# Performance work log

Hardware: AMD Instinct MI355X
Metric: run time of the kernel (lower is better)

## Reference

```python
import jax, jax.numpy as jnp
import numpy as np

K = 3  # local attention window (kernel_size)


def setup_inputs() -> dict:
    key = jax.random.key(0)
    ks = jax.random.split(key, 10)
    B, C, S = 1, 128, 24
    scale = 1.0 / np.sqrt(C).astype(np.float32)
    x = jax.random.normal(ks[0], (B, C, S, S, S), dtype=jnp.float32)
    wq = jax.random.normal(ks[1], (C, C), dtype=jnp.float32) * scale
    bq = jax.random.normal(ks[2], (C,), dtype=jnp.float32) * 0.01
    wk = jax.random.normal(ks[3], (C, C), dtype=jnp.float32) * scale
    bk = jax.random.normal(ks[4], (C,), dtype=jnp.float32) * 0.01
    wv = jax.random.normal(ks[5], (C, C), dtype=jnp.float32) * scale
    bv = jax.random.normal(ks[6], (C,), dtype=jnp.float32) * 0.01
    rel_h = jax.random.normal(ks[7], (C // 2, K, 1, 1), dtype=jnp.float32)
    rel_w = jax.random.normal(ks[8], (C // 2, 1, K, 1), dtype=jnp.float32)
    rel_d = jax.random.normal(ks[9], (C // 2, 1, 1, K), dtype=jnp.float32)
    return {"x": x, "wq": wq, "bq": bq, "wk": wk, "bk": bk,
            "wv": wv, "bv": bv, "rel_h": rel_h, "rel_w": rel_w, "rel_d": rel_d}


def reference(x, wq, bq, wk, bk, wv, bv, rel_h, rel_w, rel_d):
    B, C, H, W, D = x.shape
    p = (K - 1) // 2
    pad = ((0, 0), (0, 0), (p, K - 1 - p), (p, K - 1 - p), (p, K - 1 - p))
    xp = jnp.pad(x, pad)

    # 1x1x1 Conv3d == per-voxel linear map
    conv1 = lambda y, w, b: jnp.einsum('bchwd,oc->bohwd', y, w) + b[None, :, None, None, None]
    q = conv1(x, wq, bq)          # [B,C,H,W,D]
    kf = conv1(xp, wk, bk)        # padded
    vf = conv1(xp, wv, bv)

    def unfold(y):
        # torch unfold(2,K,1).unfold(3,K,1).unfold(4,K,1) flattened row-major (i,j,l)
        pats = [y[:, :, i:i + H, j:j + W, l:l + D]
                for i in range(K) for j in range(K) for l in range(K)]
        return jnp.stack(pats, axis=-1)  # [B,C,H,W,D,K^3]

    kw = unfold(kf)
    vw = unfold(vf)

    # q^T k per voxel over the K^3 window (num_heads=1 so head split is identity)
    qk = jnp.einsum('bchwd,bchwds->bhwds', q, kw)  # [B,H,W,D,27]

    # Faithful to einsum('bhxytdz,cijk->bhxytijk'): d,z,c are all summed
    # independently -> (sum_d q) * (sum_c rel) broadcast over the window.
    qsum = jnp.sum(q, axis=1)                         # [B,H,W,D]
    bias = rel_h.sum(0) + rel_w.sum(0) + rel_d.sum(0)  # [K,K,K] via broadcast
    qk = qk.reshape(B, H, W, D, K, K, K) + qsum[..., None, None, None] * bias

    attn = jax.nn.softmax(qk.reshape(B, H, W, D, K ** 3), axis=-1)
    out = jnp.einsum('bhwds,bchwds->bhwdc', attn, vw)  # [B,H,W,D,C]
    # torch: [B,1,H,W,D,1,C].reshape(B,-1,H,W,D) -- same row-major flatten here
    return out.reshape(B, -1, H, W, D)
```

## Files before the change

### kernel.cpp

```cpp
#include <hip/hip_runtime.h>
#include <hip/hip_fp16.h>

#define CCH 128
#define SV 24
#define NVOX 13824

typedef unsigned short u16;
typedef unsigned int   u32;

__device__ __forceinline__ void cvt8h(uint4 r, float* f) {
    const __half2* h = (const __half2*)&r;
    const float2 a = __half22float2(h[0]);
    const float2 b = __half22float2(h[1]);
    const float2 c = __half22float2(h[2]);
    const float2 d = __half22float2(h[3]);
    f[0] = a.x; f[1] = a.y; f[2] = b.x; f[3] = b.y;
    f[4] = c.x; f[5] = c.y; f[6] = d.x; f[7] = d.y;
}
__device__ __forceinline__ u32 pack2h(float a, float b) {
    const __half2 h = __floats2half2_rn(a, b);
    return *(const u32*)&h;
}

__global__ __launch_bounds__(256) void proj_kernel(
    const float* __restrict__ x,
    const float* __restrict__ wq, const float* __restrict__ bq,
    const float* __restrict__ wk, const float* __restrict__ bk,
    const float* __restrict__ wv, const float* __restrict__ bv,
    const float* __restrict__ relh, const float* __restrict__ relw,
    const float* __restrict__ reld,
    float* __restrict__ qout, u16* __restrict__ kws, u16* __restrict__ vws,
    float* __restrict__ biasW)
{
    const int m = blockIdx.y;
    const float* __restrict__ w = (m == 0) ? wq : (m == 1) ? wk : wv;
    const float* __restrict__ b = (m == 0) ? bq : (m == 1) ? bk : bv;

    __shared__ float Xs[32][64];
    __shared__ float Ws[32][128];

    const int tid  = threadIdx.x;
    const int vox0 = blockIdx.x * 64;
    const int v0   = (tid & 15) * 4;
    const int o0   = (tid >> 4) * 8;

    const int xc  = tid >> 3;
    const int xv  = (tid & 7) * 4;
    const int wo  = tid >> 1;
    const int wkh = (tid & 1) * 16;

    float acc[4][8] = {{0.f}};

    for (int k0 = 0; k0 < CCH; k0 += 32) {
        {
            const float* src = x + (size_t)(k0 + xc) * NVOX + vox0 + xv;
            const float4 a0 = *(const float4*)src;
            const float4 a1 = *(const float4*)(src + 32);
            *(float4*)&Xs[xc][xv]      = a0;
            *(float4*)&Xs[xc][xv + 32] = a1;
        }
        {
            const float* src = w + (size_t)wo * CCH + k0 + wkh;
            const float4 b0 = *(const float4*)src;
            const float4 b1 = *(const float4*)(src + 4);
            const float4 b2 = *(const float4*)(src + 8);
            const float4 b3 = *(const float4*)(src + 12);
            Ws[wkh + 0][wo] = b0.x;  Ws[wkh + 1][wo] = b0.y;
            Ws[wkh + 2][wo] = b0.z;  Ws[wkh + 3][wo] = b0.w;
            Ws[wkh + 4][wo] = b1.x;  Ws[wkh + 5][wo] = b1.y;
            Ws[wkh + 6][wo] = b1.z;  Ws[wkh + 7][wo] = b1.w;
            Ws[wkh + 8][wo] = b2.x;  Ws[wkh + 9][wo] = b2.y;
            Ws[wkh + 10][wo] = b2.z; Ws[wkh + 11][wo] = b2.w;
            Ws[wkh + 12][wo] = b3.x; Ws[wkh + 13][wo] = b3.y;
            Ws[wkh + 14][wo] = b3.z; Ws[wkh + 15][wo] = b3.w;
        }
        __syncthreads();

#pragma unroll
        for (int k = 0; k < 32; ++k) {
            const float4 xf = *(const float4*)&Xs[k][v0];
            const float4 w0 = *(const float4*)&Ws[k][o0];
            const float4 w1 = *(const float4*)&Ws[k][o0 + 4];
            const float xr[4] = {xf.x, xf.y, xf.z, xf.w};
            const float wr[8] = {w0.x, w0.y, w0.z, w0.w,
                                 w1.x, w1.y, w1.z, w1.w};
#pragma unroll
            for (int vv = 0; vv < 4; ++vv)
#pragma unroll
                for (int oo = 0; oo < 8; ++oo)
                    acc[vv][oo] = fmaf(xr[vv], wr[oo], acc[vv][oo]);
        }
        __syncthreads();
    }

    const float4 bf0 = *(const float4*)(b + o0);
    const float4 bf1 = *(const float4*)(b + o0 + 4);
    const float br[8] = {bf0.x, bf0.y, bf0.z, bf0.w,
                         bf1.x, bf1.y, bf1.z, bf1.w};

#pragma unroll
    for (int vv = 0; vv < 4; ++vv) {
        float r[8];
#pragma unroll
        for (int oo = 0; oo < 8; ++oo) r[oo] = acc[vv][oo] + br[oo];
        const size_t row = (size_t)(vox0 + v0 + vv) * CCH + o0;
        if (m == 0) {
            float4 s0 = {r[0], r[1], r[2], r[3]};
            float4 s1 = {r[4], r[5], r[6], r[7]};
            *(float4*)(qout + row) = s0;
            *(float4*)(qout + row + 4) = s1;
        } else {
            u16* out = (m == 1) ? kws : vws;
            uint4 st = {pack2h(r[0], r[1]), pack2h(r[2], r[3]),
                        pack2h(r[4], r[5]), pack2h(r[6], r[7])};
            *(uint4*)(out + row) = st;
        }
    }

    if (blockIdx.x == 0) {
        if (m == 1 && tid < CCH) {
            const __half hb = __float2half_rn(bk[tid]);
            kws[(size_t)NVOX * CCH + tid] = *(const u16*)&hb;
        }
        if (m == 2 && tid < CCH) {
            const __half hb = __float2half_rn(bv[tid]);
            vws[(size_t)NVOX * CCH + tid] = *(const u16*)&hb;
        }
        if (m == 1 && tid < 27) {
            const int i = tid / 9, j = (tid / 3) % 3, l = tid % 3;
            float s = 0.f;
            for (int c = 0; c < 64; ++c)
                s += relh[c * 3 + i] + relw[c * 3 + j] + reld[c * 3 + l];
            biasW[tid] = s;
        }
    }
}

__device__ __forceinline__ int nbr_off(int h, int w, int d, int s, int ch) {
    const int nh = h + s / 9 - 1;
    const int nw = w + (s / 3) % 3 - 1;
    const int nd = d + s % 3 - 1;
    const bool ok = ((unsigned)nh < (unsigned)SV) &&
                    ((unsigned)nw < (unsigned)SV) &&
                    ((unsigned)nd < (unsigned)SV);
    const int idx = ok ? ((nh * SV + nw) * SV + nd) : NVOX;
    return idx * CCH + ch;
}

__global__ __launch_bounds__(256) void attn_kernel(
    float* __restrict__ qo, const u16* __restrict__ kws,
    const u16* __restrict__ vws, const float* __restrict__ biasW)
{
    const int tid  = threadIdx.x;
    const int lane = tid & 15;
    const int vox  = blockIdx.x * 16 + (tid >> 4);
    const int h    = vox / 576;
    const int rem  = vox - h * 576;
    const int w    = rem / 24;
    const int d    = rem - w * 24;
    const int ch   = lane * 8;

    const float* qrow = qo + (size_t)vox * CCH + ch;
    const float4 q0 = *(const float4*)qrow;
    const float4 q1 = *(const float4*)(qrow + 4);
    const float qr[8] = {q0.x, q0.y, q0.z, q0.w, q1.x, q1.y, q1.z, q1.w};

    float qs = qr[0] + qr[1] + qr[2] + qr[3] + qr[4] + qr[5] + qr[6] + qr[7];
#pragma unroll
    for (int mm = 1; mm < 16; mm <<= 1) qs += __shfl_xor(qs, mm, 64);

    float ps[27];
#pragma unroll
    for (int sb = 0; sb < 27; sb += 9) {
        uint4 kf[9];
#pragma unroll
        for (int j = 0; j < 9; ++j)
            kf[j] = *(const uint4*)(kws + nbr_off(h, w, d, sb + j, ch));
#pragma unroll
        for (int j = 0; j < 9; ++j) {
            float f[8];
            cvt8h(kf[j], f);
            float p = qr[0] * f[0];
            p = fmaf(qr[1], f[1], p); p = fmaf(qr[2], f[2], p);
            p = fmaf(qr[3], f[3], p); p = fmaf(qr[4], f[4], p);
            p = fmaf(qr[5], f[5], p); p = fmaf(qr[6], f[6], p);
            p = fmaf(qr[7], f[7], p);
            ps[sb + j] = p;
        }
    }

#pragma unroll
    for (int mm = 1; mm < 16; mm <<= 1) {
#pragma unroll
        for (int s = 0; s < 27; ++s) ps[s] += __shfl_xor(ps[s], mm, 64);
    }

#pragma unroll
    for (int s = 0; s < 27; ++s) ps[s] = fmaf(qs, biasW[s], ps[s]);

    float mx = ps[0];
#pragma unroll
    for (int s = 1; s < 27; ++s) mx = fmaxf(mx, ps[s]);
    float sum = 0.f;
#pragma unroll
    for (int s = 0; s < 27; ++s) { ps[s] = __expf(ps[s] - mx); sum += ps[s]; }
    const float inv = 1.f / sum;
#pragma unroll
    for (int s = 0; s < 27; ++s) ps[s] *= inv;

    float o[8] = {0.f, 0.f, 0.f, 0.f, 0.f, 0.f, 0.f, 0.f};
#pragma unroll
    for (int sb = 0; sb < 27; sb += 9) {
        uint4 vf[9];
#pragma unroll
        for (int j = 0; j < 9; ++j)
            vf[j] = *(const uint4*)(vws + nbr_off(h, w, d, sb + j, ch));
#pragma unroll
        for (int j = 0; j < 9; ++j) {
            float f[8];
            cvt8h(vf[j], f);
            const float a = ps[sb + j];
#pragma unroll
            for (int e = 0; e < 8; ++e) o[e] = fmaf(a, f[e], o[e]);
        }
    }

    float* dst = qo + (size_t)vox * CCH + ch;
    float4 s0 = {o[0], o[1], o[2], o[3]};
    float4 s1 = {o[4], o[5], o[6], o[7]};
    *(float4*)dst = s0;
    *(float4*)(dst + 4) = s1;
}

extern "C" void kernel_launch(void* const* d_in, const int* in_sizes, int n_in,
                              void* d_out, int out_size, void* d_ws,
                              size_t ws_size, hipStream_t stream)
{
    const float* x    = (const float*)d_in[0];
    const float* wq   = (const float*)d_in[1];
    const float* bq   = (const float*)d_in[2];
    const float* wk   = (const float*)d_in[3];
    const float* bk   = (const float*)d_in[4];
    const float* wv   = (const float*)d_in[5];
    const float* bv   = (const float*)d_in[6];
    const float* relh = (const float*)d_in[7];
    const float* relw = (const float*)d_in[8];
    const float* reld = (const float*)d_in[9];

    u16*   kws   = (u16*)d_ws;
    u16*   vws   = kws + (size_t)(NVOX + 1) * CCH;
    float* biasW = (float*)(vws + (size_t)(NVOX + 1) * CCH);

    dim3 pgrid(NVOX / 64, 3);
    proj_kernel<<<pgrid, 256, 0, stream>>>(x, wq, bq, wk, bk, wv, bv,
                                           relh, relw, reld,
                                           (float*)d_out, kws, vws, biasW);
    attn_kernel<<<NVOX / 16, 256, 0, stream>>>((float*)d_out, kws, vws, biasW);
}
```

Baseline: 107.6 us.

## Tile attention into 4x4x2 voxel blocks with shared-memory K/V halo reuse

Rewrites the attention kernel so each block handles a 4x4x2 voxel tile. The 6x6x4 halo of K and then V is staged into LDS, which replaces 27 separate global gathers per voxel with shared reuse across neighbours. Work is reorganised so threads compute several window scores over full channels and then split the output channels. This adds syncthreads, LDS pressure and fewer blocks (432), and the softmax runs serially on only 32 threads.

```diff
diff --git a/kernel.cpp b/kernel.cpp
--- a/kernel.cpp
+++ b/kernel.cpp
@@ -136,100 +136,153 @@
     }
 }
 
-__device__ __forceinline__ int nbr_off(int h, int w, int d, int s, int ch) {
-    const int nh = h + s / 9 - 1;
-    const int nw = w + (s / 3) % 3 - 1;
-    const int nd = d + s % 3 - 1;
-    const bool ok = ((unsigned)nh < (unsigned)SV) &&
-                    ((unsigned)nw < (unsigned)SV) &&
-                    ((unsigned)nd < (unsigned)SV);
-    const int idx = ok ? ((nh * SV + nw) * SV + nd) : NVOX;
-    return idx * CCH + ch;
-}
+#define KSTR 136
+#define QSTR 132
 
 __global__ __launch_bounds__(256) void attn_kernel(
     float* __restrict__ qo, const u16* __restrict__ kws,
     const u16* __restrict__ vws, const float* __restrict__ biasW)
 {
-    const int tid  = threadIdx.x;
-    const int lane = tid & 15;
-    const int vox  = blockIdx.x * 16 + (tid >> 4);
-    const int h    = vox / 576;
-    const int rem  = vox - h * 576;
-    const int w    = rem / 24;
-    const int d    = rem - w * 24;
-    const int ch   = lane * 8;
-
-    const float* qrow = qo + (size_t)vox * CCH + ch;
-    const float4 q0 = *(const float4*)qrow;
-    const float4 q1 = *(const float4*)(qrow + 4);
-    const float qr[8] = {q0.x, q0.y, q0.z, q0.w, q1.x, q1.y, q1.z, q1.w};
-
-    float qs = qr[0] + qr[1] + qr[2] + qr[3] + qr[4] + qr[5] + qr[6] + qr[7];
-#pragma unroll
-    for (int mm = 1; mm < 16; mm <<= 1) qs += __shfl_xor(qs, mm, 64);
-
-    float ps[27];
-#pragma unroll
-    for (int sb = 0; sb < 27; sb += 9) {
-        uint4 kf[9];
-#pragma unroll
-        for (int j = 0; j < 9; ++j)
-            kf[j] = *(const uint4*)(kws + nbr_off(h, w, d, sb + j, ch));
-#pragma unroll
-        for (int j = 0; j < 9; ++j) {
+    __shared__ u16   KV[144 * KSTR];
+    __shared__ float Qs[32 * QSTR];
+    __shared__ float probs[32 * 27];
+
+    const int tid = threadIdx.x;
+    const int bx  = blockIdx.x;
+    const int th = bx / 72, rb = bx % 72, tw = rb / 12, td = rb % 12;
+    const int h0 = th * 4, w0 = tw * 4, d0 = td * 2;
+
+#pragma unroll
+    for (int it = 0; it < 9; ++it) {
+        const int e   = it * 256 + tid;
+        const int row = e >> 4, seg = e & 15;
+        const int lh = row / 24, rr = row % 24, lw = rr >> 2, ld = rr & 3;
+        const int nh = h0 + lh - 1, nw = w0 + lw - 1, nd = d0 + ld - 1;
+        const bool ok = ((unsigned)nh < 24u) && ((unsigned)nw < 24u) &&
+                        ((unsigned)nd < 24u);
+        const int gv = ok ? ((nh * 24 + nw) * 24 + nd) : NVOX;
+        const uint4 kv = *(const uint4*)(kws + (size_t)gv * CCH + seg * 8);
+        *(uint4*)&KV[row * KSTR + seg * 8] = kv;
+    }
+#pragma unroll
+    for (int it = 0; it < 4; ++it) {
+        const int e = it * 256 + tid;
+        const int v = e >> 5, seg = e & 31;
+        const int gh = h0 + (v >> 3), gw = w0 + ((v >> 1) & 3),
+                  gd = d0 + (v & 1);
+        const int gv = (gh * 24 + gw) * 24 + gd;
+        const float4 qv = *(const float4*)(qo + (size_t)gv * CCH + seg * 4);
+        *(float4*)&Qs[v * QSTR + seg * 4] = qv;
+    }
+    __syncthreads();
+
+    {
+        const int v  = tid & 31;
+        const int s0 = tid >> 5;
+        const int vh = v >> 3, vw = (v >> 1) & 3, vd = v & 1;
+        int r[4];
+#pragma unroll
+        for (int jj = 0; jj < 4; ++jj) {
+            int s = s0 + jj * 8; if (s > 26) s = 26;
+            const int i = s / 9, j = (s / 3) % 3, l = s % 3;
+            r[jj] = (vh + i) * 24 + (vw + j) * 4 + (vd + l);
+        }
+        float acc[4] = {0.f, 0.f, 0.f, 0.f};
+        for (int c = 0; c < 128; c += 8) {
+            const float4 q0 = *(const float4*)&Qs[v * QSTR + c];
+            const float4 q1 = *(const float4*)&Qs[v * QSTR + c + 4];
+            const float qr[8] = {q0.x, q0.y, q0.z, q0.w,
+                                 q1.x, q1.y, q1.z, q1.w};
+#pragma unroll
+            for (int jj = 0; jj < 4; ++jj) {
+                const uint4 kr = *(const uint4*)&KV[r[jj] * KSTR + c];
+                float f[8];
+                cvt8h(kr, f);
+                float p = acc[jj];
+                p = fmaf(qr[0], f[0], p); p = fmaf(qr[1], f[1], p);
+                p = fmaf(qr[2], f[2], p); p = fmaf(qr[3], f[3], p);
+                p = fmaf(qr[4], f[4], p); p = fmaf(qr[5], f[5], p);
+                p = fmaf(qr[6], f[6], p); p = fmaf(qr[7], f[7], p);
+                acc[jj] = p;
+            }
+        }
+#pragma unroll
+        for (int jj = 0; jj < 4; ++jj) {
+            const int s = s0 + jj * 8;
+            if (s < 27) probs[v * 27 + s] = acc[jj];
+        }
+    }
+    __syncthreads();
+
+    if (tid < 32) {
+        const int v = tid;
+        float qsum = 0.f;
+        for (int c = 0; c < 128; c += 4) {
+            const float4 q = *(const float4*)&Qs[v * QSTR + c];
+            qsum += q.x + q.y + q.z + q.w;
+        }
+        float L[27];
+        float mx = -1e30f;
+#pragma unroll
+        for (int s = 0; s < 27; ++s) {
+            L[s] = fmaf(qsum, biasW[s], probs[v * 27 + s]);
+            mx = fmaxf(mx, L[s]);
+        }
+        float sum = 0.f;
+#pragma unroll
+        for (int s = 0; s < 27; ++s) { L[s] = __expf(L[s] - mx); sum += L[s]; }
+        const float inv = 1.f / sum;
+#pragma unroll
+        for (int s = 0; s < 27; ++s) probs[v * 27 + s] = L[s] * inv;
+    }
+#pragma unroll
+    for (int it = 0; it < 9; ++it) {
+        const int e   = it * 256 + tid;
+        const int row = e >> 4, seg = e & 15;
+        const int lh = row / 24, rr = row % 24, lw = rr >> 2, ld = rr & 3;
+        const int nh = h0 + lh - 1, nw = w0 + lw - 1, nd = d0 + ld - 1;
+        const bool ok = ((unsigned)nh < 24u) && ((unsigned)nw < 24u) &&
+                        ((unsigned)nd < 24u);
+        const int gv = ok ? ((nh * 24 + nw) * 24 + nd) : NVOX;
+        const uint4 vv = *(const uint4*)(vws + (size_t)gv * CCH + seg * 8);
+        *(uint4*)&KV[row * KSTR + seg * 8] = vv;
+    }
+    __syncthreads();
+
+    {
+        const int v  = tid & 31;
+        const int cg = tid >> 5;
+        const int c0 = cg * 16;
+        const int vh = v >> 3, vw = (v >> 1) & 3, vd = v & 1;
+        float acc[16];
+#pragma unroll
+        for (int e = 0; e < 16; ++e) acc[e] = 0.f;
+
+#pragma unroll
+        for (int s = 0; s < 27; ++s) {
+            const int i = s / 9, j = (s / 3) % 3, l = s % 3;
+            const int r = (vh + i) * 24 + (vw + j) * 4 + (vd + l);
+            const float a = probs[v * 27 + s];
+            const uint4 w0 = *(const uint4*)&KV[r * KSTR + c0];
+            const uint4 w1 = *(const uint4*)&KV[r * KSTR + c0 + 8];
             float f[8];
-            cvt8h(kf[j], f);
-            float p = qr[0] * f[0];
-            p = fmaf(qr[1], f[1], p); p = fmaf(qr[2], f[2], p);
-            p = fmaf(qr[3], f[3], p); p = fmaf(qr[4], f[4], p);
-            p = fmaf(qr[5], f[5], p); p = fmaf(qr[6], f[6], p);
-            p = fmaf(qr[7], f[7], p);
-            ps[sb + j] = p;
-        }
-    }
-
-#pragma unroll
-    for (int mm = 1; mm < 16; mm <<= 1) {
-#pragma unroll
-        for (int s = 0; s < 27; ++s) ps[s] += __shfl_xor(ps[s], mm, 64);
-    }
-
-#pragma unroll
-    for (int s = 0; s < 27; ++s) ps[s] = fmaf(qs, biasW[s], ps[s]);
-
-    float mx = ps[0];
-#pragma unroll
-    for (int s = 1; s < 27; ++s) mx = fmaxf(mx, ps[s]);
-    float sum = 0.f;
-#pragma unroll
-    for (int s = 0; s < 27; ++s) { ps[s] = __expf(ps[s] - mx); sum += ps[s]; }
-    const float inv = 1.f / sum;
-#pragma unroll
-    for (int s = 0; s < 27; ++s) ps[s] *= inv;
-
-    float o[8] = {0.f, 0.f, 0.f, 0.f, 0.f, 0.f, 0.f, 0.f};
-#pragma unroll
-    for (int sb = 0; sb < 27; sb += 9) {
-        uint4 vf[9];
-#pragma unroll
-        for (int j = 0; j < 9; ++j)
-            vf[j] = *(const uint4*)(vws + nbr_off(h, w, d, sb + j, ch));
-#pragma unroll
-        for (int j = 0; j < 9; ++j) {
-            float f[8];
-            cvt8h(vf[j], f);
-            const float a = ps[sb + j];
-#pragma unroll
-            for (int e = 0; e < 8; ++e) o[e] = fmaf(a, f[e], o[e]);
-        }
-    }
-
-    float* dst = qo + (size_t)vox * CCH + ch;
-    float4 s0 = {o[0], o[1], o[2], o[3]};
-    float4 s1 = {o[4], o[5], o[6], o[7]};
-    *(float4*)dst = s0;
-    *(float4*)(dst + 4) = s1;
+            cvt8h(w0, f);
+#pragma unroll
+            for (int e = 0; e < 8; ++e) acc[e] = fmaf(a, f[e], acc[e]);
+            cvt8h(w1, f);
+#pragma unroll
+            for (int e = 0; e < 8; ++e) acc[8 + e] = fmaf(a, f[e], acc[8 + e]);
+        }
+
+        const int gh = h0 + vh, gw = w0 + vw, gd = d0 + vd;
+        float* dst = qo + (size_t)((gh * 24 + gw) * 24 + gd) * CCH + c0;
+#pragma unroll
+        for (int e = 0; e < 4; ++e) {
+            float4 st = {acc[4 * e], acc[4 * e + 1],
+                         acc[4 * e + 2], acc[4 * e + 3]};
+            *(float4*)(dst + 4 * e) = st;
+        }
+    }
 }
 
 extern "C" void kernel_launch(void* const* d_in, const int* in_sizes, int n_in,
@@ -255,5 +308,5 @@
     proj_kernel<<<pgrid, 256, 0, stream>>>(x, wq, bq, wk, bk, wv, bv,
                                            relh, relw, reld,
                                            (float*)d_out, kws, vws, biasW);
-    attn_kernel<<<NVOX / 16, 256, 0, stream>>>((float*)d_out, kws, vws, biasW);
-}
+    attn_kernel<<<432, 256, 0, stream>>>((float*)d_out, kws, vws, biasW);
+}
```

Measured after the change: 112.1 us. 4.2% more time.

## Split Q and KV projections; compute KV projection with fp16 dot2 instructions

Applied to the files above, without the earlier changes.

The single fused projection kernel becomes two: an fp32 Q projection and a K/V projection. The K/V kernel converts x and the weights to packed half pairs in shared memory and accumulates with v_dot2 (fp16 inputs, fp32 accumulate). It also issues the global loads before the barrier so they overlap with the previous iteration, and pads the shared arrays. This halves LDS traffic and FMA count for K/V, at the cost of an extra kernel launch and fp16 rounding of inputs (the outputs were already stored as fp16).

```diff
diff --git a/kernel.cpp b/kernel.cpp
--- a/kernel.cpp
+++ b/kernel.cpp
@@ -7,6 +7,7 @@
 
 typedef unsigned short u16;
 typedef unsigned int   u32;
+typedef __fp16 h2 __attribute__((ext_vector_type(2)));
 
 __device__ __forceinline__ void cvt8h(uint4 r, float* f) {
     const __half2* h = (const __half2*)&r;
@@ -21,21 +22,16 @@
     const __half2 h = __floats2half2_rn(a, b);
     return *(const u32*)&h;
 }
-
-__global__ __launch_bounds__(256) void proj_kernel(
+__device__ __forceinline__ float fdot2(u32 a, u32 b, float c) {
+    return __builtin_amdgcn_fdot2(__builtin_bit_cast(h2, a),
+                                  __builtin_bit_cast(h2, b), c, false);
+}
+
+__global__ __launch_bounds__(256) void proj_q_kernel(
     const float* __restrict__ x,
     const float* __restrict__ wq, const float* __restrict__ bq,
-    const float* __restrict__ wk, const float* __restrict__ bk,
-    const float* __restrict__ wv, const float* __restrict__ bv,
-    const float* __restrict__ relh, const float* __restrict__ relw,
-    const float* __restrict__ reld,
-    float* __restrict__ qout, u16* __restrict__ kws, u16* __restrict__ vws,
-    float* __restrict__ biasW)
+    float* __restrict__ qout)
 {
-    const int m = blockIdx.y;
-    const float* __restrict__ w = (m == 0) ? wq : (m == 1) ? wk : wv;
-    const float* __restrict__ b = (m == 0) ? bq : (m == 1) ? bk : bv;
-
     __shared__ float Xs[32][64];
     __shared__ float Ws[32][128];
 
@@ -60,7 +56,7 @@
             *(float4*)&Xs[xc][xv + 32] = a1;
         }
         {
-            const float* src = w + (size_t)wo * CCH + k0 + wkh;
+            const float* src = wq + (size_t)wo * CCH + k0 + wkh;
             const float4 b0 = *(const float4*)src;
             const float4 b1 = *(const float4*)(src + 4);
             const float4 b2 = *(const float4*)(src + 8);
@@ -93,6 +89,93 @@
         __syncthreads();
     }
 
+    const float4 bf0 = *(const float4*)(bq + o0);
+    const float4 bf1 = *(const float4*)(bq + o0 + 4);
+    const float br[8] = {bf0.x, bf0.y, bf0.z, bf0.w,
+                         bf1.x, bf1.y, bf1.z, bf1.w};
+
+#pragma unroll
+    for (int vv = 0; vv < 4; ++vv) {
+        const size_t row = (size_t)(vox0 + v0 + vv) * CCH + o0;
+        float4 s0 = {acc[vv][0] + br[0], acc[vv][1] + br[1],
+                     acc[vv][2] + br[2], acc[vv][3] + br[3]};
+        float4 s1 = {acc[vv][4] + br[4], acc[vv][5] + br[5],
+                     acc[vv][6] + br[6], acc[vv][7] + br[7]};
+        *(float4*)(qout + row) = s0;
+        *(float4*)(qout + row + 4) = s1;
+    }
+}
+
+__global__ __launch_bounds__(256) void proj_kv_kernel(
+    const float* __restrict__ x,
+    const float* __restrict__ wk, const float* __restrict__ bk,
+    const float* __restrict__ wv, const float* __restrict__ bv,
+    const float* __restrict__ relh, const float* __restrict__ relw,
+    const float* __restrict__ reld,
+    u16* __restrict__ kws, u16* __restrict__ vws, float* __restrict__ biasW)
+{
+    const int m = blockIdx.y;
+    const float* __restrict__ w = (m == 0) ? wk : wv;
+    const float* __restrict__ b = (m == 0) ? bk : bv;
+    u16* __restrict__ out       = (m == 0) ? kws : vws;
+
+    __shared__ u32 Xh[16][68];
+    __shared__ u32 Wh[16][132];
+
+    const int tid  = threadIdx.x;
+    const int vox0 = blockIdx.x * 64;
+    const int v0   = (tid & 15) * 4;
+    const int o0   = (tid >> 4) * 8;
+
+    const int cpX = tid >> 4;
+    const int vg  = (tid & 15) * 4;
+    const int wo  = tid >> 1;
+    const int cpW = (tid & 1) * 8;
+
+    float acc[4][8] = {{0.f}};
+
+    for (int k0 = 0; k0 < CCH; k0 += 32) {
+        const float* xe = x + (size_t)(k0 + 2 * cpX) * NVOX + vox0 + vg;
+        const float4 a0 = *(const float4*)xe;
+        const float4 a1 = *(const float4*)(xe + NVOX);
+        const float* wsrc = w + (size_t)wo * CCH + k0 + 2 * cpW;
+        const float4 b0 = *(const float4*)wsrc;
+        const float4 b1 = *(const float4*)(wsrc + 4);
+        const float4 b2 = *(const float4*)(wsrc + 8);
+        const float4 b3 = *(const float4*)(wsrc + 12);
+
+        __syncthreads();
+        {
+            uint4 px = {pack2h(a0.x, a1.x), pack2h(a0.y, a1.y),
+                        pack2h(a0.z, a1.z), pack2h(a0.w, a1.w)};
+            *(uint4*)&Xh[cpX][vg] = px;
+            Wh[cpW + 0][wo] = pack2h(b0.x, b0.y);
+            Wh[cpW + 1][wo] = pack2h(b0.z, b0.w);
+            Wh[cpW + 2][wo] = pack2h(b1.x, b1.y);
+            Wh[cpW + 3][wo] = pack2h(b1.z, b1.w);
+            Wh[cpW + 4][wo] = pack2h(b2.x, b2.y);
+            Wh[cpW + 5][wo] = pack2h(b2.z, b2.w);
+            Wh[cpW + 6][wo] = pack2h(b3.x, b3.y);
+            Wh[cpW + 7][wo] = pack2h(b3.z, b3.w);
+        }
+        __syncthreads();
+
+#pragma unroll
+        for (int cp = 0; cp < 16; ++cp) {
+            const uint4 xv = *(const uint4*)&Xh[cp][v0];
+            const uint4 wa = *(const uint4*)&Wh[cp][o0];
+            const uint4 wb = *(const uint4*)&Wh[cp][o0 + 4];
+            const u32 xr[4] = {xv.x, xv.y, xv.z, xv.w};
+            const u32 wr[8] = {wa.x, wa.y, wa.z, wa.w,
+                               wb.x, wb.y, wb.z, wb.w};
+#pragma unroll
+            for (int vv = 0; vv < 4; ++vv)
+#pragma unroll
+                for (int oo = 0; oo < 8; ++oo)
+                    acc[vv][oo] = fdot2(xr[vv], wr[oo], acc[vv][oo]);
+        }
+    }
+
     const float4 bf0 = *(const float4*)(b + o0);
     const float4 bf1 = *(const float4*)(b + o0 + 4);
     const float br[8] = {bf0.x, bf0.y, bf0.z, bf0.w,
@@ -104,29 +187,17 @@
 #pragma unroll
         for (int oo = 0; oo < 8; ++oo) r[oo] = acc[vv][oo] + br[oo];
         const size_t row = (size_t)(vox0 + v0 + vv) * CCH + o0;
-        if (m == 0) {
-            float4 s0 = {r[0], r[1], r[2], r[3]};
-            float4 s1 = {r[4], r[5], r[6], r[7]};
-            *(float4*)(qout + row) = s0;
-            *(float4*)(qout + row + 4) = s1;
-        } else {
-            u16* out = (m == 1) ? kws : vws;
-            uint4 st = {pack2h(r[0], r[1]), pack2h(r[2], r[3]),
-                        pack2h(r[4], r[5]), pack2h(r[6], r[7])};
-            *(uint4*)(out + row) = st;
-        }
+        uint4 st = {pack2h(r[0], r[1]), pack2h(r[2], r[3]),
+                    pack2h(r[4], r[5]), pack2h(r[6], r[7])};
+        *(uint4*)(out + row) = st;
     }
 
     if (blockIdx.x == 0) {
-        if (m == 1 && tid < CCH) {
-            const __half hb = __float2half_rn(bk[tid]);
-            kws[(size_t)NVOX * CCH + tid] = *(const u16*)&hb;
-        }
-        if (m == 2 && tid < CCH) {
-            const __half hb = __float2half_rn(bv[tid]);
-            vws[(size_t)NVOX * CCH + tid] = *(const u16*)&hb;
-        }
-        if (m == 1 && tid < 27) {
+        if (tid < CCH) {
+            const __half hb = __float2half_rn(b[tid]);
+            out[(size_t)NVOX * CCH + tid] = *(const u16*)&hb;
+        }
+        if (m == 0 && tid < 27) {
             const int i = tid / 9, j = (tid / 3) % 3, l = tid % 3;
             float s = 0.f;
             for (int c = 0; c < 64; ++c)
@@ -251,9 +322,10 @@
     u16*   vws   = kws + (size_t)(NVOX + 1) * CCH;
     float* biasW = (float*)(vws + (size_t)(NVOX + 1) * CCH);
 
-    dim3 pgrid(NVOX / 64, 3);
-    proj_kernel<<<pgrid, 256, 0, stream>>>(x, wq, bq, wk, bk, wv, bv,
-                                           relh, relw, reld,
-                                           (float*)d_out, kws, vws, biasW);
+    proj_q_kernel<<<NVOX / 64, 256, 0, stream>>>(x, wq, bq, (float*)d_out);
+    dim3 kvgrid(NVOX / 64, 2);
+    proj_kv_kernel<<<kvgrid, 256, 0, stream>>>(x, wk, bk, wv, bv,
+                                               relh, relw, reld,
+                                               kws, vws, biasW);
     attn_kernel<<<NVOX / 16, 256, 0, stream>>>((float*)d_out, kws, vws, biasW);
 }
```

Measured after the change: 116.1 us. 1.08x slower.
